# Performance work log

Hardware: AMD Instinct MI355X
Metric: run time of the kernel (lower is better)

Reference implementation:

```python
import jax, jax.numpy as jnp
import numpy as np

K = 2        # top-k experts
ALPHA = 0.01  # load-balance loss weight
BETA = 0.1    # z-router loss weight

B, T, D, E = 4, 4096, 2048, 64


def setup_inputs() -> dict:
    key = jax.random.key(0)
    kx, kw = jax.random.split(key)
    x = jax.random.normal(kx, (B, T, D), dtype=jnp.float32)
    W = jax.random.normal(kw, (D, E), dtype=jnp.float32) * (1.0 / np.sqrt(D))
    b = jnp.zeros((E,), dtype=jnp.float32)
    return {"x": x, "W": W, "b": b}


def reference(x, W, b):
    # Router logits and softmax: [B, T, E]
    logits = jnp.einsum("btd,de->bte", x, W) + b
    scores = jax.nn.softmax(logits, axis=-1)

    # Top-k selection and renormalized combine weights: [B, T, K]
    topk_vals, topk_idx = jax.lax.top_k(scores, K)
    combine = topk_vals / jnp.sum(topk_vals, axis=-1, keepdims=True)

    # Load-balance loss (Fedus et al. 2022): f_e = fraction of tokens whose
    # max score is expert e; P_e = mean prob mass on expert e.
    is_max = (scores == jnp.max(scores, axis=-1, keepdims=True)).astype(jnp.float32)
    f = jnp.mean(is_max, axis=(0, 1))   # [E]
    P = jnp.mean(scores, axis=(0, 1))   # [E]
    balance_loss = ALPHA * jnp.mean(f * P)

    # Z-router loss; faithfully applied to post-softmax scores as in source.
    lse = jax.nn.logsumexp(scores, axis=-1)  # [B, T]
    z_loss = BETA * jnp.mean(lse ** 2)

    return topk_idx, combine, balance_loss, z_loss
```

## Files before the change

kernel.cpp:

```cpp
#include <hip/hip_runtime.h>
#include <math.h>

#define NTOK 16384
#define DDIM 2048
#define NEXP 64
#define MT   16
#define KCH  128
#define NCH  (DDIM / KCH)

#define ACC_N  129
#define WF_OFF 256
#define VSTRIDE ((size_t)4 * 64 * 64 * 8)

typedef __attribute__((ext_vector_type(8))) short short8_t;
typedef __attribute__((ext_vector_type(4))) float f32x4;

__device__ __forceinline__ unsigned short f2bf(float f) {
    unsigned int u = __float_as_uint(f);
    u += 0x7fffu + ((u >> 16) & 1u);
    return (unsigned short)(u >> 16);
}
__device__ __forceinline__ float bf2f(unsigned short s) {
    return __uint_as_float(((unsigned int)s) << 16);
}

__global__ __launch_bounds__(256) void prep(
    const float* __restrict__ W, float* __restrict__ ws)
{
    const int i = blockIdx.x * 256 + threadIdx.x;
    if (blockIdx.x == 0 && threadIdx.x < ACC_N) ws[threadIdx.x] = 0.0f;
    const int k = i >> 6, e = i & 63;
    const float v = W[i];
    unsigned short h = f2bf(v);
    float r1 = v - bf2f(h);
    unsigned short m = f2bf(r1);
    unsigned short l = f2bf(r1 - bf2f(m));
    unsigned short* wf = (unsigned short*)(ws + WF_OFF);
    const int g = e >> 4, ks = k >> 5;
    const int lane = (((k >> 3) & 3) << 4) | (e & 15);
    const int j = k & 7;
    const size_t base = ((((size_t)g * 64) + ks) * 64 + lane) * 8 + j;
    wf[base] = h;
    wf[VSTRIDE + base] = m;
    wf[2 * VSTRIDE + base] = l;
}

__global__ __launch_bounds__(256, 4) void gate_fused(
    const float* __restrict__ x, const unsigned short* __restrict__ wf,
    const float* __restrict__ bias, float* __restrict__ out,
    float* __restrict__ acc_g)
{
    __shared__ __align__(16) unsigned short xh[2][MT * KCH];
    __shared__ __align__(16) unsigned short xm_[2][MT * KCH];
    __shared__ __align__(16) unsigned short xl_[2][MT * KCH];
    __shared__ float logits[MT][68];
    __shared__ int   f_loc[NEXP];
    __shared__ float p_loc[NEXP];
    __shared__ float z_loc;

    const int tid  = threadIdx.x;
    const int tok0 = blockIdx.x * MT;
    const int lane = tid & 63;
    const int g    = __builtin_amdgcn_readfirstlane(tid >> 6);

    if (tid < NEXP) { f_loc[tid] = 0; p_loc[tid] = 0.0f; }
    if (tid == 0) z_loc = 0.0f;

    const int srow = tid >> 4;
    const int scg  = tid & 15;
    const float* xs = x + (size_t)(tok0 + srow) * DDIM + scg * 8;
    const int wbase = srow * KCH;
    const int s0 = (scg ^ (srow & 7)) * 8;

    const int arow  = lane & 15;
    const int akq   = lane >> 4;
    const int abase = arow * KCH;

    f32x4 acc = {0.0f, 0.0f, 0.0f, 0.0f};

    {
        float4 a0 = *(const float4*)(xs + 0);
        float4 a1 = *(const float4*)(xs + 4);
        float xv[8];
        *(float4*)&xv[0] = a0; *(float4*)&xv[4] = a1;
        unsigned short th[8], tm[8], tl[8];
        #pragma unroll
        for (int i = 0; i < 8; ++i) {
            float f = xv[i];
            th[i] = f2bf(f);
            float r = f - bf2f(th[i]);
            tm[i] = f2bf(r);
            tl[i] = f2bf(r - bf2f(tm[i]));
        }
        *(short8_t*)&xh[0][wbase + s0]  = *(short8_t*)&th[0];
        *(short8_t*)&xm_[0][wbase + s0] = *(short8_t*)&tm[0];
        *(short8_t*)&xl_[0][wbase + s0] = *(short8_t*)&tl[0];
    }
    float4 pv0 = *(const float4*)(xs + KCH + 0);
    float4 pv1 = *(const float4*)(xs + KCH + 4);

    #pragma unroll 1
    for (int c = 0; c < NCH; ++c) {
        __syncthreads();
        const int cb = c & 1, nb = cb ^ 1;

        if (c + 1 < NCH) {
            float xv[8];
            *(float4*)&xv[0] = pv0; *(float4*)&xv[4] = pv1;
            unsigned short th[8], tm[8], tl[8];
            #pragma unroll
            for (int i = 0; i < 8; ++i) {
                float f = xv[i];
                th[i] = f2bf(f);
                float r = f - bf2f(th[i]);
                tm[i] = f2bf(r);
                tl[i] = f2bf(r - bf2f(tm[i]));
            }
            *(short8_t*)&xh[nb][wbase + s0]  = *(short8_t*)&th[0];
            *(short8_t*)&xm_[nb][wbase + s0] = *(short8_t*)&tm[0];
            *(short8_t*)&xl_[nb][wbase + s0] = *(short8_t*)&tl[0];
            if (c + 2 < NCH) {
                const float* xn = xs + (c + 2) * KCH;
                pv0 = *(const float4*)(xn + 0);
                pv1 = *(const float4*)(xn + 4);
            }
        }

        const unsigned short* wb0 =
            wf + ((((size_t)g * 64) + c * 4) * 64 + lane) * 8;
        #pragma unroll
        for (int s = 0; s < 4; ++s) {
            const int slot = (((s * 4 + akq) ^ (arow & 7))) * 8;
            short8_t ah = *(const short8_t*)&xh[cb][abase + slot];
            short8_t am = *(const short8_t*)&xm_[cb][abase + slot];
            short8_t al = *(const short8_t*)&xl_[cb][abase + slot];
            const unsigned short* wb = wb0 + (size_t)s * 64 * 8;
            short8_t bh = *(const short8_t*)&wb[0];
            short8_t bm = *(const short8_t*)&wb[VSTRIDE];
            short8_t bl = *(const short8_t*)&wb[2 * VSTRIDE];
            acc = __builtin_amdgcn_mfma_f32_16x16x32_bf16(ah, bh, acc, 0, 0, 0);
            acc = __builtin_amdgcn_mfma_f32_16x16x32_bf16(ah, bm, acc, 0, 0, 0);
            acc = __builtin_amdgcn_mfma_f32_16x16x32_bf16(am, bh, acc, 0, 0, 0);
            acc = __builtin_amdgcn_mfma_f32_16x16x32_bf16(ah, bl, acc, 0, 0, 0);
            acc = __builtin_amdgcn_mfma_f32_16x16x32_bf16(am, bm, acc, 0, 0, 0);
            acc = __builtin_amdgcn_mfma_f32_16x16x32_bf16(al, bh, acc, 0, 0, 0);
        }
    }

    #pragma unroll
    for (int r = 0; r < 4; ++r)
        logits[akq * 4 + r][g * 16 + arow] = acc[r];
    __syncthreads();

    const int tx = tid & 15;
    const int tg = tid >> 4;
    const int e0 = tx * 4;
    const int gt = tok0 + tg;

    float bb[4];
    *(float4*)bb = *(const float4*)&bias[e0];
    float l[4];
    {
        float4 lv = *(const float4*)&logits[tg][e0];
        l[0] = lv.x + bb[0]; l[1] = lv.y + bb[1];
        l[2] = lv.z + bb[2]; l[3] = lv.w + bb[3];
    }

    float v1 = l[0], v2 = -INFINITY;
    int   i1 = e0,   i2 = 0x7fffffff;
    #pragma unroll
    for (int j = 1; j < 4; ++j) {
        float v = l[j]; int e = e0 + j;
        if (v > v1)      { v2 = v1; i2 = i1; v1 = v; i1 = e; }
        else if (v > v2) { v2 = v;  i2 = e; }
    }
    #pragma unroll
    for (int off = 1; off < 16; off <<= 1) {
        float o1 = __shfl_xor(v1, off, 16); int oi1 = __shfl_xor(i1, off, 16);
        float o2 = __shfl_xor(v2, off, 16); int oi2 = __shfl_xor(i2, off, 16);
        if (o1 > v1 || (o1 == v1 && oi1 < i1)) {
            float cs = v1; int ci = i1;
            v1 = o1; i1 = oi1;
            if (cs > o2 || (cs == o2 && ci < oi2)) { v2 = cs; i2 = ci;  }
            else                                   { v2 = o2; i2 = oi2; }
        } else {
            if (o1 > v2 || (o1 == v2 && oi1 < i2)) { v2 = o1; i2 = oi1; }
        }
    }
    const float mx = v1;

    float sden[4], dsum = 0.0f;
    #pragma unroll
    for (int j = 0; j < 4; ++j) { sden[j] = __expf(l[j] - mx); dsum += sden[j]; }
    #pragma unroll
    for (int off = 1; off < 16; off <<= 1) dsum += __shfl_xor(dsum, off, 16);
    const float inv = 1.0f / dsum;

    float p[4], zsum = 0.0f;
    #pragma unroll
    for (int j = 0; j < 4; ++j) {
        p[j] = sden[j] * inv;
        zsum += __expf(p[j]);
    }
    #pragma unroll
    for (int off = 1; off < 16; off <<= 1) zsum += __shfl_xor(zsum, off, 16);

    float zacc = 0.0f;
    if (tx == 0) {
        const float s2 = __expf(v2 - mx);
        const float ci = 1.0f / (1.0f + s2);
        out[2 * gt]     = (float)i1;
        out[2 * gt + 1] = (float)i2;
        out[2 * NTOK + 2 * gt]     = ci;
        out[2 * NTOK + 2 * gt + 1] = s2 * ci;
        atomicAdd(&f_loc[i1], 1);
        float lse = __logf(zsum);
        zacc = lse * lse;
    }

    #pragma unroll
    for (int off = 1; off < 64; off <<= 1) zacc += __shfl_xor(zacc, off);
    if ((tid & 63) == 0) atomicAdd(&z_loc, zacc);

    #pragma unroll
    for (int j = 0; j < 4; ++j) {
        p[j] += __shfl_xor(p[j], 16);
        p[j] += __shfl_xor(p[j], 32);
    }
    if ((tid & 63) < 16) {
        #pragma unroll
        for (int j = 0; j < 4; ++j) atomicAdd(&p_loc[e0 + j], p[j]);
    }

    __syncthreads();
    if (tid < NEXP) {
        atomicAdd(&acc_g[64 + tid], p_loc[tid]);
        if (f_loc[tid]) atomicAdd(&acc_g[tid], (float)f_loc[tid]);
    }
    if (tid == 0) atomicAdd(&acc_g[128], z_loc);
}

__global__ void gate_finalize(const float* __restrict__ acc, float* __restrict__ out) {
    int e = threadIdx.x;
    float v = acc[e] * acc[64 + e];
    #pragma unroll
    for (int off = 32; off > 0; off >>= 1) v += __shfl_down(v, off);
    if (e == 0) {
        const float NT = (float)NTOK;
        out[2 * NTOK * 2]     = 0.01f * (v / (float)NEXP) / (NT * NT);
        out[2 * NTOK * 2 + 1] = 0.1f * acc[128] / NT;
    }
}

extern "C" void kernel_launch(void* const* d_in, const int* in_sizes, int n_in,
                              void* d_out, int out_size, void* d_ws, size_t ws_size,
                              hipStream_t stream) {
    const float* x    = (const float*)d_in[0];
    const float* W    = (const float*)d_in[1];
    const float* bias = (const float*)d_in[2];
    float* out = (float*)d_out;
    float* ws  = (float*)d_ws;
    const unsigned short* wfrag = (const unsigned short*)(ws + WF_OFF);

    prep<<<(DDIM * NEXP) / 256, 256, 0, stream>>>(W, ws);
    gate_fused<<<NTOK / MT, 256, 0, stream>>>(x, wfrag, bias, out, ws);
    gate_finalize<<<1, 64, 0, stream>>>(ws, out);
}
```

Measured before the change: 68.99 us.

## Double token tile per block, halve K chunk, split accumulators for MFMA ILP

Doubles the tokens per block to 32 and halves the K-chunk to 64. Each wave now reuses its split-bf16 W fragments across two 16-row token sub-tiles, which halves global W traffic per token and halves the block count. The six dependent MFMAs are spread across three independent accumulators per sub-tile to shorten dependency chains, and s_setprio raises wave priority around the MFMA section. The epilogue loops over two tokens per thread group. The cost is more accumulator registers and twice as many chunk iterations and barriers.

```diff
diff --git a/kernel.cpp b/kernel.cpp
--- a/kernel.cpp
+++ b/kernel.cpp
@@ -4,8 +4,8 @@
 #define NTOK 16384
 #define DDIM 2048
 #define NEXP 64
-#define MT   16
-#define KCH  128
+#define MT   32
+#define KCH  64
 #define NCH  (DDIM / KCH)
 
 #define ACC_N  129
@@ -45,6 +45,26 @@
     wf[2 * VSTRIDE + base] = l;
 }
 
+__device__ __forceinline__ void conv_store(
+    unsigned short* dh, unsigned short* dm, unsigned short* dl,
+    float4 a0, float4 a1)
+{
+    float xv[8];
+    *(float4*)&xv[0] = a0; *(float4*)&xv[4] = a1;
+    unsigned short th[8], tm[8], tl[8];
+    #pragma unroll
+    for (int i = 0; i < 8; ++i) {
+        float f = xv[i];
+        th[i] = f2bf(f);
+        float r = f - bf2f(th[i]);
+        tm[i] = f2bf(r);
+        tl[i] = f2bf(r - bf2f(tm[i]));
+    }
+    *(short8_t*)dh = *(short8_t*)&th[0];
+    *(short8_t*)dm = *(short8_t*)&tm[0];
+    *(short8_t*)dl = *(short8_t*)&tl[0];
+}
+
 __global__ __launch_bounds__(256, 4) void gate_fused(
     const float* __restrict__ x, const unsigned short* __restrict__ wf,
     const float* __restrict__ bias, float* __restrict__ out,
@@ -66,35 +86,28 @@
     if (tid < NEXP) { f_loc[tid] = 0; p_loc[tid] = 0.0f; }
     if (tid == 0) z_loc = 0.0f;
 
-    const int srow = tid >> 4;
-    const int scg  = tid & 15;
+    const int srow = tid >> 3;
+    const int scg  = tid & 7;
     const float* xs = x + (size_t)(tok0 + srow) * DDIM + scg * 8;
     const int wbase = srow * KCH;
-    const int s0 = (scg ^ (srow & 7)) * 8;
-
-    const int arow  = lane & 15;
-    const int akq   = lane >> 4;
-    const int abase = arow * KCH;
-
-    f32x4 acc = {0.0f, 0.0f, 0.0f, 0.0f};
+    const int s0 = ((scg ^ (srow & 7))) * 8;
+
+    const int arow16 = lane & 15;
+    const int akq    = lane >> 4;
+    const int asw    = arow16 & 7;
+
+    f32x4 acc[2][3];
+    #pragma unroll
+    for (int q = 0; q < 2; ++q)
+        #pragma unroll
+        for (int ch = 0; ch < 3; ++ch)
+            acc[q][ch] = (f32x4){0.f, 0.f, 0.f, 0.f};
 
     {
         float4 a0 = *(const float4*)(xs + 0);
         float4 a1 = *(const float4*)(xs + 4);
-        float xv[8];
-        *(float4*)&xv[0] = a0; *(float4*)&xv[4] = a1;
-        unsigned short th[8], tm[8], tl[8];
-        #pragma unroll
-        for (int i = 0; i < 8; ++i) {
-            float f = xv[i];
-            th[i] = f2bf(f);
-            float r = f - bf2f(th[i]);
-            tm[i] = f2bf(r);
-            tl[i] = f2bf(r - bf2f(tm[i]));
-        }
-        *(short8_t*)&xh[0][wbase + s0]  = *(short8_t*)&th[0];
-        *(short8_t*)&xm_[0][wbase + s0] = *(short8_t*)&tm[0];
-        *(short8_t*)&xl_[0][wbase + s0] = *(short8_t*)&tl[0];
+        conv_store(&xh[0][wbase + s0], &xm_[0][wbase + s0],
+                   &xl_[0][wbase + s0], a0, a1);
     }
     float4 pv0 = *(const float4*)(xs + KCH + 0);
     float4 pv1 = *(const float4*)(xs + KCH + 4);
@@ -105,20 +118,8 @@
         const int cb = c & 1, nb = cb ^ 1;
 
         if (c + 1 < NCH) {
-            float xv[8];
-            *(float4*)&xv[0] = pv0; *(float4*)&xv[4] = pv1;
-            unsigned short th[8], tm[8], tl[8];
-            #pragma unroll
-            for (int i = 0; i < 8; ++i) {
-                float f = xv[i];
-                th[i] = f2bf(f);
-                float r = f - bf2f(th[i]);
-                tm[i] = f2bf(r);
-                tl[i] = f2bf(r - bf2f(tm[i]));
-            }
-            *(short8_t*)&xh[nb][wbase + s0]  = *(short8_t*)&th[0];
-            *(short8_t*)&xm_[nb][wbase + s0] = *(short8_t*)&tm[0];
-            *(short8_t*)&xl_[nb][wbase + s0] = *(short8_t*)&tl[0];
+            conv_store(&xh[nb][wbase + s0], &xm_[nb][wbase + s0],
+                       &xl_[nb][wbase + s0], pv0, pv1);
             if (c + 2 < NCH) {
                 const float* xn = xs + (c + 2) * KCH;
                 pv0 = *(const float4*)(xn + 0);
@@ -126,96 +127,114 @@
             }
         }
 
-        const unsigned short* wb0 =
-            wf + ((((size_t)g * 64) + c * 4) * 64 + lane) * 8;
-        #pragma unroll
-        for (int s = 0; s < 4; ++s) {
-            const int slot = (((s * 4 + akq) ^ (arow & 7))) * 8;
-            short8_t ah = *(const short8_t*)&xh[cb][abase + slot];
-            short8_t am = *(const short8_t*)&xm_[cb][abase + slot];
-            short8_t al = *(const short8_t*)&xl_[cb][abase + slot];
-            const unsigned short* wb = wb0 + (size_t)s * 64 * 8;
+        __builtin_amdgcn_s_setprio(1);
+        #pragma unroll
+        for (int s = 0; s < 2; ++s) {
+            const int ks = c * 2 + s;
+            const unsigned short* wb =
+                wf + ((((size_t)g * 64) + ks) * 64 + lane) * 8;
             short8_t bh = *(const short8_t*)&wb[0];
             short8_t bm = *(const short8_t*)&wb[VSTRIDE];
             short8_t bl = *(const short8_t*)&wb[2 * VSTRIDE];
-            acc = __builtin_amdgcn_mfma_f32_16x16x32_bf16(ah, bh, acc, 0, 0, 0);
-            acc = __builtin_amdgcn_mfma_f32_16x16x32_bf16(ah, bm, acc, 0, 0, 0);
-            acc = __builtin_amdgcn_mfma_f32_16x16x32_bf16(am, bh, acc, 0, 0, 0);
-            acc = __builtin_amdgcn_mfma_f32_16x16x32_bf16(ah, bl, acc, 0, 0, 0);
-            acc = __builtin_amdgcn_mfma_f32_16x16x32_bf16(am, bm, acc, 0, 0, 0);
-            acc = __builtin_amdgcn_mfma_f32_16x16x32_bf16(al, bh, acc, 0, 0, 0);
-        }
-    }
-
-    #pragma unroll
-    for (int r = 0; r < 4; ++r)
-        logits[akq * 4 + r][g * 16 + arow] = acc[r];
+            const int slot = (((s * 4 + akq) ^ asw)) * 8;
+            #pragma unroll
+            for (int q = 0; q < 2; ++q) {
+                const int ab = (16 * q + arow16) * KCH + slot;
+                short8_t ah = *(const short8_t*)&xh[cb][ab];
+                short8_t am = *(const short8_t*)&xm_[cb][ab];
+                short8_t al = *(const short8_t*)&xl_[cb][ab];
+                acc[q][0] = __builtin_amdgcn_mfma_f32_16x16x32_bf16(ah, bh, acc[q][0], 0, 0, 0);
+                acc[q][1] = __builtin_amdgcn_mfma_f32_16x16x32_bf16(ah, bm, acc[q][1], 0, 0, 0);
+                acc[q][2] = __builtin_amdgcn_mfma_f32_16x16x32_bf16(am, bm, acc[q][2], 0, 0, 0);
+                acc[q][0] = __builtin_amdgcn_mfma_f32_16x16x32_bf16(ah, bl, acc[q][0], 0, 0, 0);
+                acc[q][1] = __builtin_amdgcn_mfma_f32_16x16x32_bf16(am, bh, acc[q][1], 0, 0, 0);
+                acc[q][2] = __builtin_amdgcn_mfma_f32_16x16x32_bf16(al, bh, acc[q][2], 0, 0, 0);
+            }
+        }
+        __builtin_amdgcn_s_setprio(0);
+    }
+
+    #pragma unroll
+    for (int q = 0; q < 2; ++q)
+        #pragma unroll
+        for (int r = 0; r < 4; ++r)
+            logits[16 * q + akq * 4 + r][g * 16 + arow16] =
+                (acc[q][0][r] + acc[q][1][r]) + acc[q][2][r];
     __syncthreads();
 
-    const int tx = tid & 15;
-    const int tg = tid >> 4;
-    const int e0 = tx * 4;
-    const int gt = tok0 + tg;
+    const int tx  = tid & 15;
+    const int tgs = tid >> 4;
+    const int e0  = tx * 4;
 
     float bb[4];
     *(float4*)bb = *(const float4*)&bias[e0];
-    float l[4];
-    {
-        float4 lv = *(const float4*)&logits[tg][e0];
-        l[0] = lv.x + bb[0]; l[1] = lv.y + bb[1];
-        l[2] = lv.z + bb[2]; l[3] = lv.w + bb[3];
-    }
-
-    float v1 = l[0], v2 = -INFINITY;
-    int   i1 = e0,   i2 = 0x7fffffff;
-    #pragma unroll
-    for (int j = 1; j < 4; ++j) {
-        float v = l[j]; int e = e0 + j;
-        if (v > v1)      { v2 = v1; i2 = i1; v1 = v; i1 = e; }
-        else if (v > v2) { v2 = v;  i2 = e; }
-    }
-    #pragma unroll
-    for (int off = 1; off < 16; off <<= 1) {
-        float o1 = __shfl_xor(v1, off, 16); int oi1 = __shfl_xor(i1, off, 16);
-        float o2 = __shfl_xor(v2, off, 16); int oi2 = __shfl_xor(i2, off, 16);
-        if (o1 > v1 || (o1 == v1 && oi1 < i1)) {
-            float cs = v1; int ci = i1;
-            v1 = o1; i1 = oi1;
-            if (cs > o2 || (cs == o2 && ci < oi2)) { v2 = cs; i2 = ci;  }
-            else                                   { v2 = o2; i2 = oi2; }
-        } else {
-            if (o1 > v2 || (o1 == v2 && oi1 < i2)) { v2 = o1; i2 = oi1; }
-        }
-    }
-    const float mx = v1;
-
-    float sden[4], dsum = 0.0f;
-    #pragma unroll
-    for (int j = 0; j < 4; ++j) { sden[j] = __expf(l[j] - mx); dsum += sden[j]; }
-    #pragma unroll
-    for (int off = 1; off < 16; off <<= 1) dsum += __shfl_xor(dsum, off, 16);
-    const float inv = 1.0f / dsum;
-
-    float p[4], zsum = 0.0f;
-    #pragma unroll
-    for (int j = 0; j < 4; ++j) {
-        p[j] = sden[j] * inv;
-        zsum += __expf(p[j]);
-    }
-    #pragma unroll
-    for (int off = 1; off < 16; off <<= 1) zsum += __shfl_xor(zsum, off, 16);
-
+
+    float pacc[4] = {0.f, 0.f, 0.f, 0.f};
     float zacc = 0.0f;
-    if (tx == 0) {
-        const float s2 = __expf(v2 - mx);
-        const float ci = 1.0f / (1.0f + s2);
-        out[2 * gt]     = (float)i1;
-        out[2 * gt + 1] = (float)i2;
-        out[2 * NTOK + 2 * gt]     = ci;
-        out[2 * NTOK + 2 * gt + 1] = s2 * ci;
-        atomicAdd(&f_loc[i1], 1);
-        float lse = __logf(zsum);
-        zacc = lse * lse;
+
+    #pragma unroll
+    for (int it = 0; it < 2; ++it) {
+        const int t  = it * 16 + tgs;
+        const int gt = tok0 + t;
+
+        float l[4];
+        {
+            float4 lv = *(const float4*)&logits[t][e0];
+            l[0] = lv.x + bb[0]; l[1] = lv.y + bb[1];
+            l[2] = lv.z + bb[2]; l[3] = lv.w + bb[3];
+        }
+
+        float v1 = l[0], v2 = -INFINITY;
+        int   i1 = e0,   i2 = 0x7fffffff;
+        #pragma unroll
+        for (int j = 1; j < 4; ++j) {
+            float v = l[j]; int e = e0 + j;
+            if (v > v1)      { v2 = v1; i2 = i1; v1 = v; i1 = e; }
+            else if (v > v2) { v2 = v;  i2 = e; }
+        }
+        #pragma unroll
+        for (int off = 1; off < 16; off <<= 1) {
+            float o1 = __shfl_xor(v1, off, 16); int oi1 = __shfl_xor(i1, off, 16);
+            float o2 = __shfl_xor(v2, off, 16); int oi2 = __shfl_xor(i2, off, 16);
+            if (o1 > v1 || (o1 == v1 && oi1 < i1)) {
+                float cs = v1; int ci = i1;
+                v1 = o1; i1 = oi1;
+                if (cs > o2 || (cs == o2 && ci < oi2)) { v2 = cs; i2 = ci;  }
+                else                                   { v2 = o2; i2 = oi2; }
+            } else {
+                if (o1 > v2 || (o1 == v2 && oi1 < i2)) { v2 = o1; i2 = oi1; }
+            }
+        }
+        const float mx = v1;
+
+        float sden[4], dsum = 0.0f;
+        #pragma unroll
+        for (int j = 0; j < 4; ++j) { sden[j] = __expf(l[j] - mx); dsum += sden[j]; }
+        #pragma unroll
+        for (int off = 1; off < 16; off <<= 1) dsum += __shfl_xor(dsum, off, 16);
+        const float inv = 1.0f / dsum;
+
+        float zsum = 0.0f;
+        #pragma unroll
+        for (int j = 0; j < 4; ++j) {
+            float pj = sden[j] * inv;
+            pacc[j] += pj;
+            zsum += __expf(pj);
+        }
+        #pragma unroll
+        for (int off = 1; off < 16; off <<= 1) zsum += __shfl_xor(zsum, off, 16);
+
+        if (tx == 0) {
+            const float s2 = __expf(v2 - mx);
+            const float ci = 1.0f / (1.0f + s2);
+            out[2 * gt]     = (float)i1;
+            out[2 * gt + 1] = (float)i2;
+            out[2 * NTOK + 2 * gt]     = ci;
+            out[2 * NTOK + 2 * gt + 1] = s2 * ci;
+            atomicAdd(&f_loc[i1], 1);
+            float lse = __logf(zsum);
+            zacc += lse * lse;
+        }
     }
 
     #pragma unroll
@@ -224,12 +243,12 @@
 
     #pragma unroll
     for (int j = 0; j < 4; ++j) {
-        p[j] += __shfl_xor(p[j], 16);
-        p[j] += __shfl_xor(p[j], 32);
+        pacc[j] += __shfl_xor(pacc[j], 16);
+        pacc[j] += __shfl_xor(pacc[j], 32);
     }
     if ((tid & 63) < 16) {
         #pragma unroll
-        for (int j = 0; j < 4; ++j) atomicAdd(&p_loc[e0 + j], p[j]);
+        for (int j = 0; j < 4; ++j) atomicAdd(&p_loc[e0 + j], pacc[j]);
     }
 
     __syncthreads();
```

Measured after the change: 65.84 us. 4.6% less time.
